# Kernel tuning notes

Measured on AMD Instinct MI355X. Metric: run time of the kernel, lower is better.

## Reference

```python
import jax, jax.numpy as jnp
import numpy as np

VOCAB = 1024
PRED_H = 320
ENC_H = 1024
JOINT_H = 640


def setup_inputs() -> dict:
    key = jax.random.key(0)
    k_f, k_g, k_w1, k_b1, k_w2, k_b2 = jax.random.split(key, 6)
    B, T, U = 8, 256, 65
    f = jax.random.normal(k_f, (B, T, ENC_H), dtype=jnp.float32)
    g = jax.random.normal(k_g, (B, U, PRED_H), dtype=jnp.float32)
    in_dim = PRED_H + ENC_H
    s1 = 1.0 / np.sqrt(in_dim)
    s2 = 1.0 / np.sqrt(JOINT_H)
    # W1 acts on cat([f, g], axis=-1): rows [0:ENC_H] hit f, rows [ENC_H:] hit g
    W1 = jax.random.uniform(k_w1, (in_dim, JOINT_H), minval=-s1, maxval=s1, dtype=jnp.float32)
    b1 = jax.random.uniform(k_b1, (JOINT_H,), minval=-s1, maxval=s1, dtype=jnp.float32)
    W2 = jax.random.uniform(k_w2, (JOINT_H, VOCAB), minval=-s2, maxval=s2, dtype=jnp.float32)
    b2 = jax.random.uniform(k_b2, (VOCAB,), minval=-s2, maxval=s2, dtype=jnp.float32)
    return {"f": f, "g": g, "W1": W1, "b1": b1, "W2": W2, "b2": b2}


def reference(f, g, W1, b1, W2, b2):
    # Linear(cat(f_expand, g_expand)) == f @ W1[:ENC_H] + g @ W1[ENC_H:] + b1,
    # broadcast-added over (T, U). Same math as the torch module (dropout p=0 / eval).
    W1f = W1[:ENC_H]          # (ENC_H, JOINT_H)
    W1g = W1[ENC_H:]          # (PRED_H, JOINT_H)
    hf = jnp.einsum("bth,hj->btj", f, W1f)            # (B, T, J)
    hg = jnp.einsum("buh,hj->buj", g, W1g)            # (B, U, J)
    h = jax.nn.relu(hf[:, :, None, :] + hg[:, None, :, :] + b1)  # (B, T, U, J)
    logits = jnp.einsum("btuj,jk->btuk", h, W2) + b2  # (B, T, U, VOCAB)
    return logits
```

## Files before the change

kernel.cpp:

```cpp
#include <hip/hip_runtime.h>
#include <cstdint>

typedef __bf16 bf16;
typedef __bf16 bf16x8 __attribute__((ext_vector_type(8)));
typedef float  f32x4  __attribute__((ext_vector_type(4)));

__global__ __launch_bounds__(256) void gemm_small(
    const float* __restrict__ A, const float* __restrict__ Bm,
    const float* __restrict__ bias, bf16* __restrict__ Cout,
    int M, int N, int K)
{
    __shared__ float As[64][20];
    __shared__ float Bs[16][68];
    const int tid = threadIdx.x;
    const int m0 = blockIdx.x * 64, n0 = blockIdx.y * 64;
    const int tx = tid & 15, ty = tid >> 4;
    const int arow = tid >> 2, ak = (tid & 3) << 2;
    const int bk = tid >> 4, bc = (tid & 15) << 2;
    const bool avalid = (m0 + arow) < M;
    float acc[4][4] = {};

    for (int k0 = 0; k0 < K; k0 += 16) {
        float4 av = make_float4(0.f, 0.f, 0.f, 0.f);
        if (avalid) av = *(const float4*)&A[(size_t)(m0 + arow) * K + k0 + ak];
        float4 bv = *(const float4*)&Bm[(size_t)(k0 + bk) * N + n0 + bc];
        __syncthreads();
        *(float4*)&As[arow][ak] = av;
        *(float4*)&Bs[bk][bc] = bv;
        __syncthreads();
#pragma unroll
        for (int k = 0; k < 16; ++k) {
            float a[4], b[4];
#pragma unroll
            for (int i = 0; i < 4; ++i) a[i] = As[ty * 4 + i][k];
#pragma unroll
            for (int j = 0; j < 4; ++j) b[j] = Bs[k][tx * 4 + j];
#pragma unroll
            for (int i = 0; i < 4; ++i)
#pragma unroll
                for (int j = 0; j < 4; ++j) acc[i][j] += a[i] * b[j];
        }
    }
#pragma unroll
    for (int i = 0; i < 4; ++i) {
        int row = m0 + ty * 4 + i;
        if (row >= M) continue;
#pragma unroll
        for (int j = 0; j < 4; ++j) {
            int col = n0 + tx * 4 + j;
            float v = acc[i][j] + (bias ? bias[col] : 0.f);
            Cout[(size_t)row * N + col] = (bf16)v;
        }
    }
}

__global__ __launch_bounds__(256) void w2_transpose(
    const float* __restrict__ W2, bf16* __restrict__ W2T)
{
    __shared__ float t[32][33];
    const int tx = threadIdx.x, ty = threadIdx.y;
    const int n0 = blockIdx.x * 32, k0 = blockIdx.y * 32;
#pragma unroll
    for (int i = 0; i < 4; ++i)
        t[ty + i * 8][tx] = W2[(size_t)(k0 + ty + i * 8) * 1024 + n0 + tx];
    __syncthreads();
#pragma unroll
    for (int i = 0; i < 4; ++i)
        W2T[(size_t)(n0 + ty + i * 8) * 640 + k0 + tx] = (bf16)t[tx][ty + i * 8];
}

__global__ __launch_bounds__(512, 2) void joint_main(
    const bf16* __restrict__ hf, const bf16* __restrict__ hgb,
    const bf16* __restrict__ W2T, const float* __restrict__ b2,
    float* __restrict__ out)
{
    __shared__ bf16 As[128 * 64];
    __shared__ bf16 Bs[256 * 64];
    const int tid = threadIdx.x;
    const int n0 = blockIdx.x * 256;
    const int m0 = blockIdx.y * 128;

    const int r  = tid >> 2;
    const int kq = (tid & 3) << 4;
    const int m  = m0 + r;
    const int bt = m / 65;
    const int uu = m - bt * 65;
    const int bb = bt >> 8;
    const bf16* hfp = hf  + (size_t)bt * 640 + kq;
    const bf16* hgp = hgb + (size_t)(bb * 65 + uu) * 640 + kq;
    const int c0 = (tid & 3) << 1;
    bf16* asw0 = &As[r * 64 + (((c0    ) ^ (r & 7)) << 3)];
    bf16* asw1 = &As[r * 64 + (((c0 + 1) ^ (r & 7)) << 3)];

    const int wid = tid >> 6, lane = tid & 63;
    const int wr = wid >> 2, wc = wid & 3;
    const int lg = lane >> 4, l15 = lane & 15;

    f32x4 acc[4][4] = {};

    for (int step = 0; step < 10; ++step) {
        const int k0 = step * 64;
        {
            const char* w2b = (const char*)W2T + (size_t)k0 * 2;
#pragma unroll
            for (int call = 0; call < 4; ++call) {
                int chunk = call * 512 + tid;
                int brow = chunk >> 3, c = chunk & 7;
                const char* src = w2b + (size_t)(n0 + brow) * 1280
                                      + ((c ^ (brow & 7)) << 4);
                __builtin_amdgcn_global_load_lds(
                    (const __attribute__((address_space(1))) uint32_t*)src,
                    (__attribute__((address_space(3))) uint32_t*)&Bs[chunk << 3],
                    16, 0, 0);
            }
        }
        {
            bf16x8 F0 = *(const bf16x8*)(hfp + k0);
            bf16x8 F1 = *(const bf16x8*)(hfp + k0 + 8);
            bf16x8 G0 = *(const bf16x8*)(hgp + k0);
            bf16x8 G1 = *(const bf16x8*)(hgp + k0 + 8);
            bf16x8 O0, O1;
#pragma unroll
            for (int i = 0; i < 8; ++i) {
                float s = (float)F0[i] + (float)G0[i];
                O0[i] = (bf16)fmaxf(s, 0.f);
            }
#pragma unroll
            for (int i = 0; i < 8; ++i) {
                float s = (float)F1[i] + (float)G1[i];
                O1[i] = (bf16)fmaxf(s, 0.f);
            }
            *(bf16x8*)asw0 = O0;
            *(bf16x8*)asw1 = O1;
        }
        __syncthreads();
#pragma unroll
        for (int kk = 0; kk < 2; ++kk) {
            const int clog = (kk << 2) + lg;
            bf16x8 afr[4], bfr[4];
#pragma unroll
            for (int mi = 0; mi < 4; ++mi) {
                int row = wr * 64 + mi * 16 + l15;
                afr[mi] = *(const bf16x8*)&As[row * 64 + ((clog ^ (row & 7)) << 3)];
            }
#pragma unroll
            for (int ni = 0; ni < 4; ++ni) {
                int row = wc * 64 + ni * 16 + l15;
                bfr[ni] = *(const bf16x8*)&Bs[row * 64 + ((clog ^ (row & 7)) << 3)];
            }
#pragma unroll
            for (int mi = 0; mi < 4; ++mi)
#pragma unroll
                for (int ni = 0; ni < 4; ++ni)
                    acc[mi][ni] = __builtin_amdgcn_mfma_f32_16x16x32_bf16(
                        afr[mi], bfr[ni], acc[mi][ni], 0, 0, 0);
        }
        __syncthreads();
    }

    float bv[4];
#pragma unroll
    for (int ni = 0; ni < 4; ++ni) bv[ni] = b2[n0 + wc * 64 + ni * 16 + l15];
#pragma unroll
    for (int mi = 0; mi < 4; ++mi) {
#pragma unroll
        for (int ni = 0; ni < 4; ++ni) {
            int col = n0 + wc * 64 + ni * 16 + l15;
#pragma unroll
            for (int j = 0; j < 4; ++j) {
                int row = m0 + wr * 64 + mi * 16 + lg * 4 + j;
                out[(size_t)row * 1024 + col] = acc[mi][ni][j] + bv[ni];
            }
        }
    }
}

extern "C" void kernel_launch(void* const* d_in, const int* in_sizes, int n_in,
                              void* d_out, int out_size, void* d_ws, size_t ws_size,
                              hipStream_t stream)
{
    const float* f  = (const float*)d_in[0];
    const float* g  = (const float*)d_in[1];
    const float* W1 = (const float*)d_in[2];
    const float* b1 = (const float*)d_in[3];
    const float* W2 = (const float*)d_in[4];
    const float* b2 = (const float*)d_in[5];
    float* out = (float*)d_out;

    bf16* hf  = (bf16*)d_ws;
    bf16* hgb = hf + 2048 * 640;
    bf16* W2T = hgb + 520 * 640;

    gemm_small<<<dim3(32, 10), 256, 0, stream>>>(f, W1, nullptr, hf, 2048, 640, 1024);
    gemm_small<<<dim3(9, 10), 256, 0, stream>>>(g, W1 + 1024 * 640, b1, hgb, 520, 640, 320);
    w2_transpose<<<dim3(32, 20), dim3(32, 8), 0, stream>>>(W2, W2T);
    joint_main<<<dim3(4, 1040), 512, 0, stream>>>(hf, hgb, W2T, b2, out);
}
```

Before: 333.3 us.

## Double-buffer joint GEMM LDS and enlarge M tile to 256 rows

Result: slower. 389.5 us (+16.8%).

```diff
diff --git a/kernel.cpp b/kernel.cpp
--- a/kernel.cpp
+++ b/kernel.cpp
@@ -74,87 +74,111 @@
     const bf16* __restrict__ W2T, const float* __restrict__ b2,
     float* __restrict__ out)
 {
-    __shared__ bf16 As[128 * 64];
-    __shared__ bf16 Bs[256 * 64];
+    __shared__ bf16 As[2][256 * 64];
+    __shared__ bf16 Bs[2][256 * 64];
     const int tid = threadIdx.x;
     const int n0 = blockIdx.x * 256;
-    const int m0 = blockIdx.y * 128;
+    const int m0 = blockIdx.y * 256;
 
     const int r  = tid >> 2;
     const int kq = (tid & 3) << 4;
-    const int m  = m0 + r;
-    const int bt = m / 65;
-    const int uu = m - bt * 65;
-    const int bb = bt >> 8;
-    const bf16* hfp = hf  + (size_t)bt * 640 + kq;
-    const bf16* hgp = hgb + (size_t)(bb * 65 + uu) * 640 + kq;
     const int c0 = (tid & 3) << 1;
-    bf16* asw0 = &As[r * 64 + (((c0    ) ^ (r & 7)) << 3)];
-    bf16* asw1 = &As[r * 64 + (((c0 + 1) ^ (r & 7)) << 3)];
+    const int aoff0 = r * 64 + (((c0    ) ^ (r & 7)) << 3);
+    const int aoff1 = r * 64 + (((c0 + 1) ^ (r & 7)) << 3);
+
+    const bf16* hfp[2];
+    const bf16* hgp[2];
+#pragma unroll
+    for (int h = 0; h < 2; ++h) {
+        int m = m0 + h * 128 + r;
+        int bt = m / 65;
+        int uu = m - bt * 65;
+        int bb = bt >> 8;
+        hfp[h] = hf  + (size_t)bt * 640 + kq;
+        hgp[h] = hgb + (size_t)(bb * 65 + uu) * 640 + kq;
+    }
 
     const int wid = tid >> 6, lane = tid & 63;
     const int wr = wid >> 2, wc = wid & 3;
     const int lg = lane >> 4, l15 = lane & 15;
 
-    f32x4 acc[4][4] = {};
-
-    for (int step = 0; step < 10; ++step) {
-        const int k0 = step * 64;
-        {
-            const char* w2b = (const char*)W2T + (size_t)k0 * 2;
-#pragma unroll
-            for (int call = 0; call < 4; ++call) {
-                int chunk = call * 512 + tid;
-                int brow = chunk >> 3, c = chunk & 7;
-                const char* src = w2b + (size_t)(n0 + brow) * 1280
-                                      + ((c ^ (brow & 7)) << 4);
-                __builtin_amdgcn_global_load_lds(
-                    (const __attribute__((address_space(1))) uint32_t*)src,
-                    (__attribute__((address_space(3))) uint32_t*)&Bs[chunk << 3],
-                    16, 0, 0);
-            }
-        }
-        {
-            bf16x8 F0 = *(const bf16x8*)(hfp + k0);
-            bf16x8 F1 = *(const bf16x8*)(hfp + k0 + 8);
-            bf16x8 G0 = *(const bf16x8*)(hgp + k0);
-            bf16x8 G1 = *(const bf16x8*)(hgp + k0 + 8);
+    bf16x8 F0[2], F1[2], G0[2], G1[2];
+
+    auto loadA = [&](int k0) {
+#pragma unroll
+        for (int h = 0; h < 2; ++h) {
+            F0[h] = *(const bf16x8*)(hfp[h] + k0);
+            F1[h] = *(const bf16x8*)(hfp[h] + k0 + 8);
+            G0[h] = *(const bf16x8*)(hgp[h] + k0);
+            G1[h] = *(const bf16x8*)(hgp[h] + k0 + 8);
+        }
+    };
+    auto stageB = [&](int buf, int k0) {
+        const char* w2b = (const char*)W2T + (size_t)k0 * 2;
+#pragma unroll
+        for (int call = 0; call < 4; ++call) {
+            int chunk = call * 512 + tid;
+            int brow = chunk >> 3, c = chunk & 7;
+            const char* src = w2b + (size_t)(n0 + brow) * 1280
+                                  + ((c ^ (brow & 7)) << 4);
+            __builtin_amdgcn_global_load_lds(
+                (const __attribute__((address_space(1))) uint32_t*)src,
+                (__attribute__((address_space(3))) uint32_t*)&Bs[buf][chunk << 3],
+                16, 0, 0);
+        }
+    };
+    auto genA = [&](int buf) {
+#pragma unroll
+        for (int h = 0; h < 2; ++h) {
             bf16x8 O0, O1;
 #pragma unroll
             for (int i = 0; i < 8; ++i) {
-                float s = (float)F0[i] + (float)G0[i];
+                float s = (float)F0[h][i] + (float)G0[h][i];
                 O0[i] = (bf16)fmaxf(s, 0.f);
             }
 #pragma unroll
             for (int i = 0; i < 8; ++i) {
-                float s = (float)F1[i] + (float)G1[i];
+                float s = (float)F1[h][i] + (float)G1[h][i];
                 O1[i] = (bf16)fmaxf(s, 0.f);
             }
-            *(bf16x8*)asw0 = O0;
-            *(bf16x8*)asw1 = O1;
-        }
-        __syncthreads();
+            *(bf16x8*)&As[buf][h * 128 * 64 + aoff0] = O0;
+            *(bf16x8*)&As[buf][h * 128 * 64 + aoff1] = O1;
+        }
+    };
+
+    f32x4 acc[8][4] = {};
+
+    loadA(0);
+    stageB(0, 0);
+    genA(0);
+    __syncthreads();
+
+    for (int t = 0; t < 10; ++t) {
+        const int cur = t & 1;
+        if (t < 9) {
+            loadA((t + 1) * 64);
+            stageB(cur ^ 1, (t + 1) * 64);
+        }
 #pragma unroll
         for (int kk = 0; kk < 2; ++kk) {
             const int clog = (kk << 2) + lg;
-            bf16x8 afr[4], bfr[4];
-#pragma unroll
-            for (int mi = 0; mi < 4; ++mi) {
-                int row = wr * 64 + mi * 16 + l15;
-                afr[mi] = *(const bf16x8*)&As[row * 64 + ((clog ^ (row & 7)) << 3)];
-            }
+            bf16x8 bfr[4];
 #pragma unroll
             for (int ni = 0; ni < 4; ++ni) {
                 int row = wc * 64 + ni * 16 + l15;
-                bfr[ni] = *(const bf16x8*)&Bs[row * 64 + ((clog ^ (row & 7)) << 3)];
-            }
-#pragma unroll
-            for (int mi = 0; mi < 4; ++mi)
+                bfr[ni] = *(const bf16x8*)&Bs[cur][row * 64 + ((clog ^ (row & 7)) << 3)];
+            }
+#pragma unroll
+            for (int mi = 0; mi < 8; ++mi) {
+                int row = wr * 128 + mi * 16 + l15;
+                bf16x8 a = *(const bf16x8*)&As[cur][row * 64 + ((clog ^ (row & 7)) << 3)];
 #pragma unroll
                 for (int ni = 0; ni < 4; ++ni)
                     acc[mi][ni] = __builtin_amdgcn_mfma_f32_16x16x32_bf16(
-                        afr[mi], bfr[ni], acc[mi][ni], 0, 0, 0);
-        }
+                        a, bfr[ni], acc[mi][ni], 0, 0, 0);
+            }
+        }
+        if (t < 9) genA(cur ^ 1);
         __syncthreads();
     }
 
@@ -162,13 +186,13 @@
 #pragma unroll
     for (int ni = 0; ni < 4; ++ni) bv[ni] = b2[n0 + wc * 64 + ni * 16 + l15];
 #pragma unroll
-    for (int mi = 0; mi < 4; ++mi) {
+    for (int mi = 0; mi < 8; ++mi) {
 #pragma unroll
         for (int ni = 0; ni < 4; ++ni) {
             int col = n0 + wc * 64 + ni * 16 + l15;
 #pragma unroll
             for (int j = 0; j < 4; ++j) {
-                int row = m0 + wr * 64 + mi * 16 + lg * 4 + j;
+                int row = m0 + wr * 128 + mi * 16 + lg * 4 + j;
                 out[(size_t)row * 1024 + col] = acc[mi][ni][j] + bv[ni];
             }
         }
@@ -194,5 +218,5 @@
     gemm_small<<<dim3(32, 10), 256, 0, stream>>>(f, W1, nullptr, hf, 2048, 640, 1024);
     gemm_small<<<dim3(9, 10), 256, 0, stream>>>(g, W1 + 1024 * 640, b1, hgb, 520, 640, 320);
     w2_transpose<<<dim3(32, 20), dim3(32, 8), 0, stream>>>(W2, W2T);
-    joint_main<<<dim3(4, 1040), 512, 0, stream>>>(hf, hgb, W2T, b2, out);
-}
+    joint_main<<<dim3(4, 520), 512, 0, stream>>>(hf, hgb, W2T, b2, out);
+}
```

## Software-pipeline joint GEMM A/B loads and merge prep kernels into one launch

Applied to the files above, without the earlier changes.

After: 426.6 us. +28.0%, slower.

```diff
diff --git a/kernel.cpp b/kernel.cpp
--- a/kernel.cpp
+++ b/kernel.cpp
@@ -5,15 +5,19 @@
 typedef __bf16 bf16x8 __attribute__((ext_vector_type(8)));
 typedef float  f32x4  __attribute__((ext_vector_type(4)));
 
-__global__ __launch_bounds__(256) void gemm_small(
+#define BARRIER()    asm volatile("s_barrier" ::: "memory")
+#define WAIT_LGKM0() asm volatile("s_waitcnt lgkmcnt(0)" ::: "memory")
+#define WAIT_VM(n)   asm volatile("s_waitcnt vmcnt(" #n ")" ::: "memory")
+
+__device__ void gemm_small_body(
     const float* __restrict__ A, const float* __restrict__ Bm,
     const float* __restrict__ bias, bf16* __restrict__ Cout,
-    int M, int N, int K)
+    int M, int N, int K, int bx, int by)
 {
     __shared__ float As[64][20];
     __shared__ float Bs[16][68];
     const int tid = threadIdx.x;
-    const int m0 = blockIdx.x * 64, n0 = blockIdx.y * 64;
+    const int m0 = bx * 64, n0 = by * 64;
     const int tx = tid & 15, ty = tid >> 4;
     const int arow = tid >> 2, ak = (tid & 3) << 2;
     const int bk = tid >> 4, bc = (tid & 15) << 2;
@@ -54,12 +58,12 @@
     }
 }
 
-__global__ __launch_bounds__(256) void w2_transpose(
-    const float* __restrict__ W2, bf16* __restrict__ W2T)
+__device__ void w2t_body(const float* __restrict__ W2, bf16* __restrict__ W2T,
+                         int bx, int by)
 {
     __shared__ float t[32][33];
-    const int tx = threadIdx.x, ty = threadIdx.y;
-    const int n0 = blockIdx.x * 32, k0 = blockIdx.y * 32;
+    const int tx = threadIdx.x & 31, ty = threadIdx.x >> 5;
+    const int n0 = bx * 32, k0 = by * 32;
 #pragma unroll
     for (int i = 0; i < 4; ++i)
         t[ty + i * 8][tx] = W2[(size_t)(k0 + ty + i * 8) * 1024 + n0 + tx];
@@ -69,7 +73,25 @@
         W2T[(size_t)(n0 + ty + i * 8) * 640 + k0 + tx] = (bf16)t[tx][ty + i * 8];
 }
 
-__global__ __launch_bounds__(512, 2) void joint_main(
+__global__ __launch_bounds__(256) void prep(
+    const float* __restrict__ f, const float* __restrict__ g,
+    const float* __restrict__ W1, const float* __restrict__ b1,
+    const float* __restrict__ W2,
+    bf16* __restrict__ hf, bf16* __restrict__ hgb, bf16* __restrict__ W2T)
+{
+    const int bid = blockIdx.x;
+    if (bid < 320) {
+        gemm_small_body(f, W1, nullptr, hf, 2048, 640, 1024, bid % 32, bid / 32);
+    } else if (bid < 410) {
+        int b = bid - 320;
+        gemm_small_body(g, W1 + 1024 * 640, b1, hgb, 520, 640, 320, b % 9, b / 9);
+    } else {
+        int b = bid - 410;
+        w2t_body(W2, W2T, b % 32, b / 32);
+    }
+}
+
+__global__ __launch_bounds__(512) void joint_main(
     const bf16* __restrict__ hf, const bf16* __restrict__ hgb,
     const bf16* __restrict__ W2T, const float* __restrict__ b2,
     float* __restrict__ out)
@@ -82,15 +104,16 @@
 
     const int r  = tid >> 2;
     const int kq = (tid & 3) << 4;
+    const int c0 = (tid & 3) << 1;
+    const int aoff0 = r * 64 + (((c0    ) ^ (r & 7)) << 3);
+    const int aoff1 = r * 64 + (((c0 + 1) ^ (r & 7)) << 3);
+
     const int m  = m0 + r;
     const int bt = m / 65;
     const int uu = m - bt * 65;
     const int bb = bt >> 8;
     const bf16* hfp = hf  + (size_t)bt * 640 + kq;
     const bf16* hgp = hgb + (size_t)(bb * 65 + uu) * 640 + kq;
-    const int c0 = (tid & 3) << 1;
-    bf16* asw0 = &As[r * 64 + (((c0    ) ^ (r & 7)) << 3)];
-    bf16* asw1 = &As[r * 64 + (((c0 + 1) ^ (r & 7)) << 3)];
 
     const int wid = tid >> 6, lane = tid & 63;
     const int wr = wid >> 2, wc = wid & 3;
@@ -98,64 +121,91 @@
 
     f32x4 acc[4][4] = {};
 
-    for (int step = 0; step < 10; ++step) {
-        const int k0 = step * 64;
-        {
-            const char* w2b = (const char*)W2T + (size_t)k0 * 2;
-#pragma unroll
-            for (int call = 0; call < 4; ++call) {
-                int chunk = call * 512 + tid;
-                int brow = chunk >> 3, c = chunk & 7;
-                const char* src = w2b + (size_t)(n0 + brow) * 1280
-                                      + ((c ^ (brow & 7)) << 4);
-                __builtin_amdgcn_global_load_lds(
-                    (const __attribute__((address_space(1))) uint32_t*)src,
-                    (__attribute__((address_space(3))) uint32_t*)&Bs[chunk << 3],
-                    16, 0, 0);
-            }
-        }
-        {
-            bf16x8 F0 = *(const bf16x8*)(hfp + k0);
-            bf16x8 F1 = *(const bf16x8*)(hfp + k0 + 8);
-            bf16x8 G0 = *(const bf16x8*)(hgp + k0);
-            bf16x8 G1 = *(const bf16x8*)(hgp + k0 + 8);
-            bf16x8 O0, O1;
-#pragma unroll
-            for (int i = 0; i < 8; ++i) {
-                float s = (float)F0[i] + (float)G0[i];
-                O0[i] = (bf16)fmaxf(s, 0.f);
-            }
-#pragma unroll
-            for (int i = 0; i < 8; ++i) {
-                float s = (float)F1[i] + (float)G1[i];
-                O1[i] = (bf16)fmaxf(s, 0.f);
-            }
-            *(bf16x8*)asw0 = O0;
-            *(bf16x8*)asw1 = O1;
-        }
-        __syncthreads();
+    auto loadA = [&](int k0, bf16x8& F0, bf16x8& F1, bf16x8& G0, bf16x8& G1) {
+        F0 = *(const bf16x8*)(hfp + k0);
+        F1 = *(const bf16x8*)(hfp + k0 + 8);
+        G0 = *(const bf16x8*)(hgp + k0);
+        G1 = *(const bf16x8*)(hgp + k0 + 8);
+    };
+    auto stageB = [&](int k0) {
+        const char* w2b = (const char*)W2T + (size_t)k0 * 2;
+#pragma unroll
+        for (int call = 0; call < 4; ++call) {
+            int chunk = call * 512 + tid;
+            int brow = chunk >> 3, c = chunk & 7;
+            const char* src = w2b + (size_t)(n0 + brow) * 1280
+                                  + ((c ^ (brow & 7)) << 4);
+            __builtin_amdgcn_global_load_lds(
+                (const __attribute__((address_space(1))) uint32_t*)src,
+                (__attribute__((address_space(3))) uint32_t*)&Bs[chunk << 3],
+                16, 0, 0);
+        }
+    };
+    auto genA = [&](const bf16x8& F0, const bf16x8& F1,
+                    const bf16x8& G0, const bf16x8& G1) {
+        bf16x8 O0, O1;
+#pragma unroll
+        for (int i = 0; i < 8; ++i) {
+            float s = (float)F0[i] + (float)G0[i];
+            O0[i] = (bf16)fmaxf(s, 0.f);
+        }
+#pragma unroll
+        for (int i = 0; i < 8; ++i) {
+            float s = (float)F1[i] + (float)G1[i];
+            O1[i] = (bf16)fmaxf(s, 0.f);
+        }
+        *(bf16x8*)&As[aoff0] = O0;
+        *(bf16x8*)&As[aoff1] = O1;
+    };
+    auto mfmaPhase = [&]() {
 #pragma unroll
         for (int kk = 0; kk < 2; ++kk) {
             const int clog = (kk << 2) + lg;
-            bf16x8 afr[4], bfr[4];
+            bf16x8 bfr[4], afr[4];
+#pragma unroll
+            for (int ni = 0; ni < 4; ++ni) {
+                int row = wc * 64 + ni * 16 + l15;
+                bfr[ni] = *(const bf16x8*)&Bs[row * 64 + ((clog ^ (row & 7)) << 3)];
+            }
 #pragma unroll
             for (int mi = 0; mi < 4; ++mi) {
                 int row = wr * 64 + mi * 16 + l15;
                 afr[mi] = *(const bf16x8*)&As[row * 64 + ((clog ^ (row & 7)) << 3)];
             }
 #pragma unroll
-            for (int ni = 0; ni < 4; ++ni) {
-                int row = wc * 64 + ni * 16 + l15;
-                bfr[ni] = *(const bf16x8*)&Bs[row * 64 + ((clog ^ (row & 7)) << 3)];
-            }
-#pragma unroll
             for (int mi = 0; mi < 4; ++mi)
 #pragma unroll
                 for (int ni = 0; ni < 4; ++ni)
                     acc[mi][ni] = __builtin_amdgcn_mfma_f32_16x16x32_bf16(
                         afr[mi], bfr[ni], acc[mi][ni], 0, 0, 0);
         }
-        __syncthreads();
+    };
+
+    bf16x8 Fa0, Fa1, Ga0, Ga1;
+    bf16x8 Fb0, Fb1, Gb0, Gb1;
+
+    loadA(0, Fa0, Fa1, Ga0, Ga1);
+    stageB(0);
+
+#pragma unroll 1
+    for (int tt = 0; tt < 5; ++tt) {
+        const int t0 = tt * 2;
+        if (t0 + 1 < 10) loadA((t0 + 1) * 64, Fb0, Fb1, Gb0, Gb1);
+        genA(Fa0, Fa1, Ga0, Ga1);
+        WAIT_VM(8);
+        WAIT_LGKM0();
+        BARRIER();
+        mfmaPhase();
+        BARRIER();
+        if (t0 + 1 < 10) stageB((t0 + 1) * 64);
+        if (t0 + 2 < 10) loadA((t0 + 2) * 64, Fa0, Fa1, Ga0, Ga1);
+        genA(Fb0, Fb1, Gb0, Gb1);
+        if (t0 + 2 < 10) { WAIT_VM(8); } else { WAIT_VM(0); }
+        WAIT_LGKM0();
+        BARRIER();
+        mfmaPhase();
+        BARRIER();
+        if (t0 + 2 < 10) stageB((t0 + 2) * 64);
     }
 
     float bv[4];
@@ -191,8 +241,6 @@
     bf16* hgb = hf + 2048 * 640;
     bf16* W2T = hgb + 520 * 640;
 
-    gemm_small<<<dim3(32, 10), 256, 0, stream>>>(f, W1, nullptr, hf, 2048, 640, 1024);
-    gemm_small<<<dim3(9, 10), 256, 0, stream>>>(g, W1 + 1024 * 640, b1, hgb, 520, 640, 320);
-    w2_transpose<<<dim3(32, 20), dim3(32, 8), 0, stream>>>(W2, W2T);
+    prep<<<1050, 256, 0, stream>>>(f, g, W1, b1, W2, hf, hgb, W2T);
     joint_main<<<dim3(4, 1040), 512, 0, stream>>>(hf, hgb, W2T, b2, out);
 }
```
